# Kernel tuning notes

Measured on AMD Instinct MI355X. Metric: run time of the kernel, lower is better.

The kernel has to match this reference:

```python
import jax, jax.numpy as jnp
import numpy as np

CUTOFF = 5.0
N_RBF = 20

A = 50000
F = 128
E = 500000


def setup_inputs() -> dict:
    key = jax.random.key(0)
    ks = jax.random.split(key, 10)
    return {
        "vectors": jax.random.normal(ks[0], (A, 3, F), dtype=jnp.float32),
        "scalars": jax.random.normal(ks[1], (A, 1, F), dtype=jnp.float32),
        "directions": jax.random.normal(ks[2], (E, 3), dtype=jnp.float32),
        "idx_i": jax.random.randint(ks[3], (E,), 0, A),
        "idx_j": jax.random.randint(ks[4], (E,), 0, A),
        "W1": jax.random.normal(ks[5], (F, F), dtype=jnp.float32) / np.sqrt(F),
        "b1": jnp.zeros((F,), dtype=jnp.float32),
        "W2": jax.random.normal(ks[6], (F, 3 * F), dtype=jnp.float32) / np.sqrt(F),
        "b2": jnp.zeros((3 * F,), dtype=jnp.float32),
        "Wr": jax.random.normal(ks[7], (N_RBF, 3 * F), dtype=jnp.float32) / np.sqrt(N_RBF),
        "br": jnp.zeros((3 * F,), dtype=jnp.float32),
    }


def reference(vectors, scalars, directions, idx_i, idx_j, W1, b1, W2, b2, Wr, br):
    feat = scalars.shape[-1]
    n_nodes = vectors.shape[0]
    n_rbf = Wr.shape[0]

    s = jax.nn.silu(scalars @ W1 + b1) @ W2 + b2

    # edge norms: E x 1
    norm_r = jnp.sqrt(jnp.sum(directions * directions, axis=-1, keepdims=True))

    # radial basis: sin(k*pi/rc * |r|)/|r|  -> E x n
    rr = jnp.arange(1, n_rbf + 1, dtype=directions.dtype)
    rbf = jnp.sin(rr * (jnp.pi / CUTOFF) * norm_r) / norm_r
    r = rbf @ Wr + br  # E x 3F

    # cosine cutoff with hard mask (min(delta,0)/delta == 1 inside cutoff, 0 outside)
    delta = norm_r - CUTOFF
    mask = jnp.minimum(delta, 0.0) / delta
    fc = 0.5 * (jnp.cos(jnp.pi * norm_r / CUTOFF) + 1.0) * mask
    r = fc * r  # E x 3F

    combined = s[idx_i] * r[:, None, :]
    delta_s, delta_v1, delta_v2 = jnp.split(combined, 3, axis=-1)

    delta_v = vectors[idx_i] * delta_v1 + delta_v2 * (directions / norm_r)[:, :, None]

    # scatter-add back to nodes
    delta_s = jax.ops.segment_sum(delta_s, idx_j, num_segments=n_nodes)
    delta_v = jax.ops.segment_sum(delta_v, idx_j, num_segments=n_nodes)
    return delta_v, delta_s
```

## Files before the change

kernel.cpp:

```cpp
#include <hip/hip_runtime.h>
#include <math.h>

#define A_NODES 50000
#define FEAT 128
#define EDGES 500000
#define NRBF 20
#define CUTOFF_F 5.0f
#define PI_OVER_CUTOFF 0.6283185307179586f

typedef unsigned int uint32;
typedef unsigned short ushort16;
typedef short bf16x8 __attribute__((ext_vector_type(8)));
typedef float f32x4 __attribute__((ext_vector_type(4)));
typedef float f32x2 __attribute__((ext_vector_type(2)));

__device__ __forceinline__ ushort16 f2bf(float f) {
    union { float f; uint32 u; } v; v.f = f;
    uint32 r = (v.u + 0x7fffu + ((v.u >> 16) & 1u)) >> 16;
    return (ushort16)r;
}
__device__ __forceinline__ uint32 packbf(float a, float b) {
    return (uint32)f2bf(a) | ((uint32)f2bf(b) << 16);
}
__device__ __forceinline__ float bf_lo(uint32 u) { return __uint_as_float(u << 16); }
__device__ __forceinline__ float bf_hi(uint32 u) { return __uint_as_float(u & 0xffff0000u); }

#if __has_builtin(__builtin_amdgcn_fdot2_f32_bf16)
typedef __bf16 bf16x2 __attribute__((ext_vector_type(2)));
__device__ __forceinline__ float dot2(uint32 a, uint32 b, float c) {
    return __builtin_amdgcn_fdot2_f32_bf16(
        __builtin_bit_cast(bf16x2, a), __builtin_bit_cast(bf16x2, b), c, false);
}
#else
__device__ __forceinline__ float dot2(uint32 a, uint32 b, float c) {
    return fmaf(bf_hi(a), bf_hi(b), fmaf(bf_lo(a), bf_lo(b), c));
}
#endif

__global__ __launch_bounds__(256) void pack_kernel(
    const float* __restrict__ W1, const float* __restrict__ W2,
    const float* __restrict__ Wr,
    ushort16* __restrict__ w1pk, ushort16* __restrict__ w2pk,
    uint32* __restrict__ wrpk)
{
    const int t = blockIdx.x * 256 + threadIdx.x;
    if (t < 16384) {
        const int jj = t & 7, l = (t >> 3) & 63, kk = (t >> 9) & 3, nt = t >> 11;
        const int col = (l & 15) + 16 * nt;
        const int k   = kk * 32 + (l >> 4) * 8 + jj;
        w1pk[t] = f2bf(W1[k * 128 + col]);
    } else if (t < 16384 + 49152) {
        const int u = t - 16384;
        const int jj = u & 7, l = (u >> 3) & 63, kk = (u >> 9) & 3, nt = u >> 11;
        const int col = (l & 15) + 16 * nt;
        const int k   = kk * 32 + (l >> 4) * 8 + jj;
        w2pk[u] = f2bf(W2[k * 384 + col]);
    } else if (t < 16384 + 49152 + 3840) {
        const int u = t - 16384 - 49152;
        const int m = u / 384, col = u % 384;
        wrpk[u] = packbf(Wr[(2 * m) * 384 + col], Wr[(2 * m + 1) * 384 + col]);
    }
}

__global__ __launch_bounds__(256) void node_mlp_kernel(
    const float* __restrict__ scalars,
    const ushort16* __restrict__ w1pk, const float* __restrict__ bias1,
    const ushort16* __restrict__ w2pk, const float* __restrict__ bias2,
    ushort16* __restrict__ s_bf)
{
    __shared__ ushort16 sc[16][136];
    __shared__ ushort16 hd[16][136];
    const int tx   = threadIdx.x;
    const int lane = tx & 63;
    const int wv   = tx >> 6;
    const int base = blockIdx.x * 16;

    {
        const int row = tx >> 4;
        const int cs  = (tx & 15) * 8;
        const float* src = scalars + (size_t)(base + row) * FEAT + cs;
        const float4 f0 = *(const float4*)src;
        const float4 f1 = *(const float4*)(src + 4);
        bf16x8 tmp;
        tmp[0] = (short)f2bf(f0.x); tmp[1] = (short)f2bf(f0.y);
        tmp[2] = (short)f2bf(f0.z); tmp[3] = (short)f2bf(f0.w);
        tmp[4] = (short)f2bf(f1.x); tmp[5] = (short)f2bf(f1.y);
        tmp[6] = (short)f2bf(f1.z); tmp[7] = (short)f2bf(f1.w);
        *(bf16x8*)&sc[row][cs] = tmp;
    }
    __syncthreads();

    const int arow = lane & 15;
    const int kgrp = lane >> 4;

    f32x4 acc0 = {0.f, 0.f, 0.f, 0.f};
    f32x4 acc1 = {0.f, 0.f, 0.f, 0.f};
    #pragma unroll
    for (int kk = 0; kk < 4; ++kk) {
        const bf16x8 a  = *(const bf16x8*)&sc[arow][kk * 32 + kgrp * 8];
        const bf16x8 b0 = *(const bf16x8*)(w1pk + (((size_t)(wv * 2 + 0) * 4 + kk) * 64 + lane) * 8);
        const bf16x8 b1 = *(const bf16x8*)(w1pk + (((size_t)(wv * 2 + 1) * 4 + kk) * 64 + lane) * 8);
        acc0 = __builtin_amdgcn_mfma_f32_16x16x32_bf16(a, b0, acc0, 0, 0, 0);
        acc1 = __builtin_amdgcn_mfma_f32_16x16x32_bf16(a, b1, acc1, 0, 0, 0);
    }
    {
        const int c0 = wv * 32 + (lane & 15);
        const int c1 = c0 + 16;
        const float bb0 = bias1[c0], bb1 = bias1[c1];
        #pragma unroll
        for (int r = 0; r < 4; ++r) {
            const int row = kgrp * 4 + r;
            float x0 = acc0[r] + bb0;
            float x1 = acc1[r] + bb1;
            x0 = x0 / (1.0f + __expf(-x0));
            x1 = x1 / (1.0f + __expf(-x1));
            hd[row][c0] = f2bf(x0);
            hd[row][c1] = f2bf(x1);
        }
    }
    __syncthreads();

    f32x4 acc[6];
    #pragma unroll
    for (int n = 0; n < 6; ++n) acc[n] = (f32x4){0.f, 0.f, 0.f, 0.f};
    #pragma unroll
    for (int kk = 0; kk < 4; ++kk) {
        const bf16x8 a = *(const bf16x8*)&hd[arow][kk * 32 + kgrp * 8];
        #pragma unroll
        for (int n = 0; n < 6; ++n) {
            const bf16x8 b = *(const bf16x8*)(w2pk + (((size_t)(wv * 6 + n) * 4 + kk) * 64 + lane) * 8);
            acc[n] = __builtin_amdgcn_mfma_f32_16x16x32_bf16(a, b, acc[n], 0, 0, 0);
        }
    }
    #pragma unroll
    for (int n = 0; n < 6; ++n) {
        const int col = (wv * 6 + n) * 16 + (lane & 15);
        const float bb = bias2[col];
        #pragma unroll
        for (int r = 0; r < 4; ++r) {
            const int row = kgrp * 4 + r;
            s_bf[(size_t)(base + row) * 384 + col] = f2bf(acc[n][r] + bb);
        }
    }
}

__global__ __launch_bounds__(256) void vec_cvt_kernel(
    const float* __restrict__ vin, uint32* __restrict__ vbf)
{
    const int t = blockIdx.x * 256 + threadIdx.x;
    const size_t n2 = (size_t)A_NODES * 384 / 2;
    if (t < (int)n2) {
        const float a = vin[2 * (size_t)t];
        const float b = vin[2 * (size_t)t + 1];
        vbf[t] = packbf(a, b);
    }
}

__global__ __launch_bounds__(256) void hist_kernel(
    const int* __restrict__ idx_j, int* __restrict__ hist)
{
    const int e = blockIdx.x * 256 + threadIdx.x;
    if (e < EDGES) atomicAdd(&hist[idx_j[e]], 1);
}

__global__ __launch_bounds__(1024) void scan_kernel(
    const int* __restrict__ hist, int* __restrict__ offsets,
    int* __restrict__ cursor)
{
    __shared__ int part[1024];
    const int t = threadIdx.x;
    const int CH = (A_NODES + 1023) / 1024;

    int sum = 0;
    for (int k = 0; k < CH; ++k) {
        const int idx = t * CH + k;
        if (idx < A_NODES) sum += hist[idx];
    }
    part[t] = sum;
    __syncthreads();
    for (int off = 1; off < 1024; off <<= 1) {
        const int v = (t >= off) ? part[t - off] : 0;
        __syncthreads();
        part[t] += v;
        __syncthreads();
    }
    int run = part[t] - sum;
    for (int k = 0; k < CH; ++k) {
        const int idx = t * CH + k;
        if (idx < A_NODES) {
            offsets[idx] = run;
            cursor[idx]  = run;
            run += hist[idx];
        }
    }
    if (t == 0) offsets[A_NODES] = EDGES;
}

__global__ __launch_bounds__(256) void edge_prep_kernel(
    const float* __restrict__ directions,
    const int* __restrict__ idx_i, const int* __restrict__ idx_j,
    int* __restrict__ cursor,
    float* __restrict__ edata)
{
    const int e = blockIdx.x * 256 + threadIdx.x;
    if (e >= EDGES) return;
    const int j   = idx_j[e];
    const int pos = atomicAdd(&cursor[j], 1);
    const int i   = idx_i[e];
    const float d0 = directions[(size_t)e * 3 + 0];
    const float d1 = directions[(size_t)e * 3 + 1];
    const float d2 = directions[(size_t)e * 3 + 2];
    const float nr   = sqrtf(d0 * d0 + d1 * d1 + d2 * d2);
    const float invn = 1.0f / nr;
    const float x = PI_OVER_CUTOFF * nr;
    float sx, cx;
    sincosf(x, &sx, &cx);
    const float fc = (nr < CUTOFF_F) ? 0.5f * (cx + 1.0f) : 0.0f;
    const float scale = invn * fc;
    const float twoc = 2.0f * cx;

    float out16[16];
    float s_odd = sx;
    float s_prev = 0.0f;
    #pragma unroll
    for (int m = 0; m < 10; ++m) {
        const float s_even = twoc * s_odd - s_prev;
        out16[m] = __uint_as_float(packbf(s_odd * scale, s_even * scale));
        const float s_next = twoc * s_even - s_odd;
        s_prev = s_even;
        s_odd  = s_next;
    }
    out16[10] = d0 * invn;
    out16[11] = d1 * invn;
    out16[12] = d2 * invn;
    out16[13] = fc;
    out16[14] = __int_as_float(i);
    out16[15] = 0.0f;

    float4* dst = (float4*)(edata + (size_t)pos * 16);
    dst[0] = make_float4(out16[0],  out16[1],  out16[2],  out16[3]);
    dst[1] = make_float4(out16[4],  out16[5],  out16[6],  out16[7]);
    dst[2] = make_float4(out16[8],  out16[9],  out16[10], out16[11]);
    dst[3] = make_float4(out16[12], out16[13], out16[14], out16[15]);
}

template <int VBF>
__global__ __launch_bounds__(256, 4) void gather_kernel(
    const ushort16* __restrict__ s_bf,
    const ushort16* __restrict__ v_bf,
    const float* __restrict__ vectors_f32,
    const uint32* __restrict__ wrpk, const float* __restrict__ br,
    const float* __restrict__ edata,
    const int* __restrict__ offsets,
    float* __restrict__ out_v, float* __restrict__ out_s)
{
    const int lane = threadIdx.x & 63;
    const int wv   = __builtin_amdgcn_readfirstlane(threadIdx.x >> 6);
    const int j    = blockIdx.x;
    const int c0   = lane * 2;

    const int beg = offsets[j];
    const int end = offsets[j + 1];

    float accsA = 0.f, accsB = 0.f;
    float avA0 = 0.f, avA1 = 0.f, avA2 = 0.f;
    float avB0 = 0.f, avB1 = 0.f, avB2 = 0.f;

    uint32 wA[30], wB[30];
    float brA0 = 0.f, brB0 = 0.f, brA1 = 0.f, brB1 = 0.f, brA2 = 0.f, brB2 = 0.f;

    int p = beg + wv;
    float4 cA, cB, cC, cD;

    if (p < end) {
        #pragma unroll
        for (int s = 0; s < 3; ++s)
            #pragma unroll
            for (int m = 0; m < 10; ++m) {
                wA[s * 10 + m] = wrpk[m * 384 + s * 128 + c0];
                wB[s * 10 + m] = wrpk[m * 384 + s * 128 + c0 + 1];
            }
        brA0 = br[c0];       brB0 = br[c0 + 1];
        brA1 = br[128 + c0]; brB1 = br[129 + c0];
        brA2 = br[256 + c0]; brB2 = br[257 + c0];

        const float4* s0p = (const float4*)(edata + (size_t)p * 16);
        cA = s0p[0]; cB = s0p[1]; cC = s0p[2]; cD = s0p[3];
    }

    while (p < end) {
        const int pn = p + 4;
        const int i  = __float_as_int(cD.z);

        const ushort16* srow = s_bf + (size_t)i * 384;
        const uint32 s0 = *(const uint32*)(srow + c0);
        const uint32 s1 = *(const uint32*)(srow + 128 + c0);
        const uint32 s2 = *(const uint32*)(srow + 256 + c0);

        float vA0, vB0, vA1, vB1, vA2, vB2;
        if (VBF) {
            const ushort16* vrow = v_bf + (size_t)i * 384;
            const uint32 v0 = *(const uint32*)(vrow + c0);
            const uint32 v1 = *(const uint32*)(vrow + 128 + c0);
            const uint32 v2 = *(const uint32*)(vrow + 256 + c0);
            vA0 = bf_lo(v0); vB0 = bf_hi(v0);
            vA1 = bf_lo(v1); vB1 = bf_hi(v1);
            vA2 = bf_lo(v2); vB2 = bf_hi(v2);
        } else {
            const float* vrow = vectors_f32 + (size_t)i * 384;
            vA0 = vrow[c0];       vB0 = vrow[c0 + 1];
            vA1 = vrow[128 + c0]; vB1 = vrow[129 + c0];
            vA2 = vrow[256 + c0]; vB2 = vrow[257 + c0];
        }

        const size_t pf = (size_t)(pn < end ? pn : p) * 16;
        const float4* sn = (const float4*)(edata + pf);
        const float4 nA = sn[0], nB = sn[1], nC = sn[2], nD = sn[3];

        const float u0 = cC.z, u1 = cC.w, u2 = cD.x;
        const float fcv = cD.y;

        uint32 rb[10] = {
            __float_as_uint(cA.x), __float_as_uint(cA.y),
            __float_as_uint(cA.z), __float_as_uint(cA.w),
            __float_as_uint(cB.x), __float_as_uint(cB.y),
            __float_as_uint(cB.z), __float_as_uint(cB.w),
            __float_as_uint(cC.x), __float_as_uint(cC.y) };

        float rA0 = fcv * brA0, rA1 = fcv * brA1, rA2 = fcv * brA2;
        float rB0 = fcv * brB0, rB1 = fcv * brB1, rB2 = fcv * brB2;
        #pragma unroll
        for (int m = 0; m < 10; ++m) {
            const uint32 rm = rb[m];
            rA0 = dot2(rm, wA[m],      rA0);
            rA1 = dot2(rm, wA[10 + m], rA1);
            rA2 = dot2(rm, wA[20 + m], rA2);
            rB0 = dot2(rm, wB[m],      rB0);
            rB1 = dot2(rm, wB[10 + m], rB1);
            rB2 = dot2(rm, wB[20 + m], rB2);
        }

        const float sA0 = bf_lo(s0), sB0 = bf_hi(s0);
        const float sA1 = bf_lo(s1), sB1 = bf_hi(s1);
        const float sA2 = bf_lo(s2), sB2 = bf_hi(s2);

        accsA = fmaf(sA0, rA0, accsA);
        accsB = fmaf(sB0, rB0, accsB);
        const float gA1 = sA1 * rA1, gA2 = sA2 * rA2;
        const float gB1 = sB1 * rB1, gB2 = sB2 * rB2;

        avA0 = fmaf(vA0, gA1, fmaf(gA2, u0, avA0));
        avB0 = fmaf(vB0, gB1, fmaf(gB2, u0, avB0));
        avA1 = fmaf(vA1, gA1, fmaf(gA2, u1, avA1));
        avB1 = fmaf(vB1, gB1, fmaf(gB2, u1, avB1));
        avA2 = fmaf(vA2, gA1, fmaf(gA2, u2, avA2));
        avB2 = fmaf(vB2, gB1, fmaf(gB2, u2, avB2));

        cA = nA; cB = nB; cC = nC; cD = nD;
        p = pn;
    }

    __shared__ float red[4][64][9];
    float* slot = red[wv][lane];
    slot[0] = accsA; slot[1] = accsB;
    slot[2] = avA0;  slot[3] = avB0;
    slot[4] = avA1;  slot[5] = avB1;
    slot[6] = avA2;  slot[7] = avB2;
    __syncthreads();

    if (wv == 0) {
        const float* o1 = red[1][lane];
        const float* o2 = red[2][lane];
        const float* o3 = red[3][lane];
        f32x2 t;
        t.x = accsA + o1[0] + o2[0] + o3[0];
        t.y = accsB + o1[1] + o2[1] + o3[1];
        __builtin_nontemporal_store(t, (f32x2*)(out_s + (size_t)j * 128 + c0));
        float* ov = out_v + (size_t)j * 384;
        t.x = avA0 + o1[2] + o2[2] + o3[2];
        t.y = avB0 + o1[3] + o2[3] + o3[3];
        __builtin_nontemporal_store(t, (f32x2*)(ov + c0));
        t.x = avA1 + o1[4] + o2[4] + o3[4];
        t.y = avB1 + o1[5] + o2[5] + o3[5];
        __builtin_nontemporal_store(t, (f32x2*)(ov + 128 + c0));
        t.x = avA2 + o1[6] + o2[6] + o3[6];
        t.y = avB2 + o1[7] + o2[7] + o3[7];
        __builtin_nontemporal_store(t, (f32x2*)(ov + 256 + c0));
    }
}

extern "C" void kernel_launch(void* const* d_in, const int* in_sizes, int n_in,
                              void* d_out, int out_size, void* d_ws, size_t ws_size,
                              hipStream_t stream) {
    const float* vectors    = (const float*)d_in[0];
    const float* scalars    = (const float*)d_in[1];
    const float* directions = (const float*)d_in[2];
    const int*   idx_i      = (const int*)d_in[3];
    const int*   idx_j      = (const int*)d_in[4];
    const float* W1         = (const float*)d_in[5];
    const float* b1         = (const float*)d_in[6];
    const float* W2         = (const float*)d_in[7];
    const float* b2         = (const float*)d_in[8];
    const float* Wr         = (const float*)d_in[9];
    const float* br         = (const float*)d_in[10];

    float* out_v = (float*)d_out;
    float* out_s = out_v + (size_t)A_NODES * 3 * FEAT;

    char* ws = (char*)d_ws;
    ushort16* s_bf = (ushort16*)ws;  ws += (size_t)A_NODES * 384 * 2;
    float* edata   = (float*)ws;     ws += (size_t)EDGES * 16 * 4;
    uint32* wrpk   = (uint32*)ws;    ws += (size_t)10 * 384 * 4;
    ushort16* w1pk = (ushort16*)ws;  ws += (size_t)16384 * 2;
    ushort16* w2pk = (ushort16*)ws;  ws += (size_t)49152 * 2;
    int* hist      = (int*)ws;       ws += (size_t)A_NODES * 4;
    int* offsets   = (int*)ws;       ws += (((size_t)(A_NODES + 1) * 4 + 15) & ~(size_t)15);
    int* cursor    = (int*)ws;       ws += (size_t)A_NODES * 4;
    ushort16* v_bf = (ushort16*)ws;  ws += (size_t)A_NODES * 384 * 2;

    const int use_vbf = ((size_t)(ws - (char*)d_ws) <= ws_size) ? 1 : 0;

    hipMemsetAsync(hist, 0, (size_t)A_NODES * 4, stream);

    pack_kernel<<<271, 256, 0, stream>>>(W1, W2, Wr, w1pk, w2pk, wrpk);
    node_mlp_kernel<<<A_NODES / 16, 256, 0, stream>>>(scalars, w1pk, b1, w2pk, b2, s_bf);
    if (use_vbf)
        vec_cvt_kernel<<<(A_NODES * 384 / 2 + 255) / 256, 256, 0, stream>>>(vectors, (uint32*)v_bf);

    hist_kernel<<<(EDGES + 255) / 256, 256, 0, stream>>>(idx_j, hist);
    scan_kernel<<<1, 1024, 0, stream>>>(hist, offsets, cursor);
    edge_prep_kernel<<<(EDGES + 255) / 256, 256, 0, stream>>>(
        directions, idx_i, idx_j, cursor, edata);

    if (use_vbf)
        gather_kernel<1><<<A_NODES, 256, 0, stream>>>(
            s_bf, v_bf, vectors, wrpk, br, edata, offsets, out_v, out_s);
    else
        gather_kernel<0><<<A_NODES, 256, 0, stream>>>(
            s_bf, v_bf, vectors, wrpk, br, edata, offsets, out_v, out_s);
}
```

Measured before the change: 613.2 us.

## Assign one wavefront per destination node and vectorize bf16 conversion

The gather kernel now maps each wavefront to its own destination node (four nodes per block) instead of splitting a node's edges across four waves. This removes the shared-memory reduction and the __syncthreads. Weight loads become vectorized uint2 and are hoisted ahead of the edge loop. The vector-to-bf16 conversion kernel is widened to process eight floats per thread with float4 loads and uint4 stores. The trade-off is a longer serial edge chain per wave and more load imbalance between waves of a block, since nodes have different degrees.

```diff
diff --git a/kernel.cpp b/kernel.cpp
--- a/kernel.cpp
+++ b/kernel.cpp
@@ -145,14 +145,17 @@
 }
 
 __global__ __launch_bounds__(256) void vec_cvt_kernel(
-    const float* __restrict__ vin, uint32* __restrict__ vbf)
-{
-    const int t = blockIdx.x * 256 + threadIdx.x;
-    const size_t n2 = (size_t)A_NODES * 384 / 2;
-    if (t < (int)n2) {
-        const float a = vin[2 * (size_t)t];
-        const float b = vin[2 * (size_t)t + 1];
-        vbf[t] = packbf(a, b);
+    const float* __restrict__ vin, uint4* __restrict__ vbf)
+{
+    const size_t t = (size_t)blockIdx.x * 256 + threadIdx.x;
+    const size_t n8 = (size_t)A_NODES * 384 / 8;
+    if (t < n8) {
+        const float4 f0 = ((const float4*)vin)[2 * t];
+        const float4 f1 = ((const float4*)vin)[2 * t + 1];
+        uint4 o;
+        o.x = packbf(f0.x, f0.y); o.y = packbf(f0.z, f0.w);
+        o.z = packbf(f1.x, f1.y); o.w = packbf(f1.z, f1.w);
+        vbf[t] = o;
     }
 }
 
@@ -255,9 +258,21 @@
     float* __restrict__ out_v, float* __restrict__ out_s)
 {
     const int lane = threadIdx.x & 63;
-    const int wv   = __builtin_amdgcn_readfirstlane(threadIdx.x >> 6);
-    const int j    = blockIdx.x;
+    const int wv   = threadIdx.x >> 6;
+    const int j    = blockIdx.x * 4 + wv;
     const int c0   = lane * 2;
+
+#define LDW(s, m) (*(const uint2*)(wrpk + (m) * 384 + (s) * 128 + c0))
+    const uint2 w00 = LDW(0,0), w01 = LDW(0,1), w02 = LDW(0,2), w03 = LDW(0,3), w04 = LDW(0,4);
+    const uint2 w05 = LDW(0,5), w06 = LDW(0,6), w07 = LDW(0,7), w08 = LDW(0,8), w09 = LDW(0,9);
+    const uint2 w10 = LDW(1,0), w11 = LDW(1,1), w12 = LDW(1,2), w13 = LDW(1,3), w14 = LDW(1,4);
+    const uint2 w15 = LDW(1,5), w16 = LDW(1,6), w17 = LDW(1,7), w18 = LDW(1,8), w19 = LDW(1,9);
+    const uint2 w20 = LDW(2,0), w21 = LDW(2,1), w22 = LDW(2,2), w23 = LDW(2,3), w24 = LDW(2,4);
+    const uint2 w25 = LDW(2,5), w26 = LDW(2,6), w27 = LDW(2,7), w28 = LDW(2,8), w29 = LDW(2,9);
+#undef LDW
+    const float2 brv0 = *(const float2*)(br + c0);
+    const float2 brv1 = *(const float2*)(br + 128 + c0);
+    const float2 brv2 = *(const float2*)(br + 256 + c0);
 
     const int beg = offsets[j];
     const int end = offsets[j + 1];
@@ -266,30 +281,15 @@
     float avA0 = 0.f, avA1 = 0.f, avA2 = 0.f;
     float avB0 = 0.f, avB1 = 0.f, avB2 = 0.f;
 
-    uint32 wA[30], wB[30];
-    float brA0 = 0.f, brB0 = 0.f, brA1 = 0.f, brB1 = 0.f, brA2 = 0.f, brB2 = 0.f;
-
-    int p = beg + wv;
+    int p = beg;
     float4 cA, cB, cC, cD;
-
     if (p < end) {
-        #pragma unroll
-        for (int s = 0; s < 3; ++s)
-            #pragma unroll
-            for (int m = 0; m < 10; ++m) {
-                wA[s * 10 + m] = wrpk[m * 384 + s * 128 + c0];
-                wB[s * 10 + m] = wrpk[m * 384 + s * 128 + c0 + 1];
-            }
-        brA0 = br[c0];       brB0 = br[c0 + 1];
-        brA1 = br[128 + c0]; brB1 = br[129 + c0];
-        brA2 = br[256 + c0]; brB2 = br[257 + c0];
-
         const float4* s0p = (const float4*)(edata + (size_t)p * 16);
         cA = s0p[0]; cB = s0p[1]; cC = s0p[2]; cD = s0p[3];
     }
 
     while (p < end) {
-        const int pn = p + 4;
+        const int pn = p + 1;
         const int i  = __float_as_int(cD.z);
 
         const ushort16* srow = s_bf + (size_t)i * 384;
@@ -317,28 +317,32 @@
         const float4* sn = (const float4*)(edata + pf);
         const float4 nA = sn[0], nB = sn[1], nC = sn[2], nD = sn[3];
 
-        const float u0 = cC.z, u1 = cC.w, u2 = cD.x;
-        const float fcv = cD.y;
-
-        uint32 rb[10] = {
-            __float_as_uint(cA.x), __float_as_uint(cA.y),
-            __float_as_uint(cA.z), __float_as_uint(cA.w),
-            __float_as_uint(cB.x), __float_as_uint(cB.y),
-            __float_as_uint(cB.z), __float_as_uint(cB.w),
-            __float_as_uint(cC.x), __float_as_uint(cC.y) };
-
-        float rA0 = fcv * brA0, rA1 = fcv * brA1, rA2 = fcv * brA2;
-        float rB0 = fcv * brB0, rB1 = fcv * brB1, rB2 = fcv * brB2;
-        #pragma unroll
-        for (int m = 0; m < 10; ++m) {
-            const uint32 rm = rb[m];
-            rA0 = dot2(rm, wA[m],      rA0);
-            rA1 = dot2(rm, wA[10 + m], rA1);
-            rA2 = dot2(rm, wA[20 + m], rA2);
-            rB0 = dot2(rm, wB[m],      rB0);
-            rB1 = dot2(rm, wB[10 + m], rB1);
-            rB2 = dot2(rm, wB[20 + m], rB2);
-        }
+        const uint32 b0 = __float_as_uint(cA.x), b1 = __float_as_uint(cA.y);
+        const uint32 b2 = __float_as_uint(cA.z), b3 = __float_as_uint(cA.w);
+        const uint32 b4 = __float_as_uint(cB.x), b5 = __float_as_uint(cB.y);
+        const uint32 b6 = __float_as_uint(cB.z), b7 = __float_as_uint(cB.w);
+        const uint32 b8 = __float_as_uint(cC.x), b9 = __float_as_uint(cC.y);
+        const float u0 = cC.z, u1 = cC.w, u2 = cD.x, fcv = cD.y;
+
+        float rA0 = fcv * brv0.x, rB0 = fcv * brv0.y;
+        float rA1 = fcv * brv1.x, rB1 = fcv * brv1.y;
+        float rA2 = fcv * brv2.x, rB2 = fcv * brv2.y;
+
+#define DOTS(bb, wa, wb, wc) \
+        rA0 = dot2(bb, wa.x, rA0); rB0 = dot2(bb, wa.y, rB0); \
+        rA1 = dot2(bb, wb.x, rA1); rB1 = dot2(bb, wb.y, rB1); \
+        rA2 = dot2(bb, wc.x, rA2); rB2 = dot2(bb, wc.y, rB2);
+        DOTS(b0, w00, w10, w20)
+        DOTS(b1, w01, w11, w21)
+        DOTS(b2, w02, w12, w22)
+        DOTS(b3, w03, w13, w23)
+        DOTS(b4, w04, w14, w24)
+        DOTS(b5, w05, w15, w25)
+        DOTS(b6, w06, w16, w26)
+        DOTS(b7, w07, w17, w27)
+        DOTS(b8, w08, w18, w28)
+        DOTS(b9, w09, w19, w29)
+#undef DOTS
 
         const float sA0 = bf_lo(s0), sB0 = bf_hi(s0);
         const float sA1 = bf_lo(s1), sB1 = bf_hi(s1);
@@ -360,33 +364,16 @@
         p = pn;
     }
 
-    __shared__ float red[4][64][9];
-    float* slot = red[wv][lane];
-    slot[0] = accsA; slot[1] = accsB;
-    slot[2] = avA0;  slot[3] = avB0;
-    slot[4] = avA1;  slot[5] = avB1;
-    slot[6] = avA2;  slot[7] = avB2;
-    __syncthreads();
-
-    if (wv == 0) {
-        const float* o1 = red[1][lane];
-        const float* o2 = red[2][lane];
-        const float* o3 = red[3][lane];
-        f32x2 t;
-        t.x = accsA + o1[0] + o2[0] + o3[0];
-        t.y = accsB + o1[1] + o2[1] + o3[1];
-        __builtin_nontemporal_store(t, (f32x2*)(out_s + (size_t)j * 128 + c0));
-        float* ov = out_v + (size_t)j * 384;
-        t.x = avA0 + o1[2] + o2[2] + o3[2];
-        t.y = avB0 + o1[3] + o2[3] + o3[3];
-        __builtin_nontemporal_store(t, (f32x2*)(ov + c0));
-        t.x = avA1 + o1[4] + o2[4] + o3[4];
-        t.y = avB1 + o1[5] + o2[5] + o3[5];
-        __builtin_nontemporal_store(t, (f32x2*)(ov + 128 + c0));
-        t.x = avA2 + o1[6] + o2[6] + o3[6];
-        t.y = avB2 + o1[7] + o2[7] + o3[7];
-        __builtin_nontemporal_store(t, (f32x2*)(ov + 256 + c0));
-    }
+    f32x2 t;
+    t.x = accsA; t.y = accsB;
+    __builtin_nontemporal_store(t, (f32x2*)(out_s + (size_t)j * 128 + c0));
+    float* ov = out_v + (size_t)j * 384;
+    t.x = avA0; t.y = avB0;
+    __builtin_nontemporal_store(t, (f32x2*)(ov + c0));
+    t.x = avA1; t.y = avB1;
+    __builtin_nontemporal_store(t, (f32x2*)(ov + 128 + c0));
+    t.x = avA2; t.y = avB2;
+    __builtin_nontemporal_store(t, (f32x2*)(ov + 256 + c0));
 }
 
 extern "C" void kernel_launch(void* const* d_in, const int* in_sizes, int n_in,
@@ -425,7 +412,8 @@
     pack_kernel<<<271, 256, 0, stream>>>(W1, W2, Wr, w1pk, w2pk, wrpk);
     node_mlp_kernel<<<A_NODES / 16, 256, 0, stream>>>(scalars, w1pk, b1, w2pk, b2, s_bf);
     if (use_vbf)
-        vec_cvt_kernel<<<(A_NODES * 384 / 2 + 255) / 256, 256, 0, stream>>>(vectors, (uint32*)v_bf);
+        vec_cvt_kernel<<<(int)(((size_t)A_NODES * 384 / 8 + 255) / 256), 256, 0, stream>>>(
+            vectors, (uint4*)v_bf);
 
     hist_kernel<<<(EDGES + 255) / 256, 256, 0, stream>>>(idx_j, hist);
     scan_kernel<<<1, 1024, 0, stream>>>(hist, offsets, cursor);
@@ -433,9 +421,9 @@
         directions, idx_i, idx_j, cursor, edata);
 
     if (use_vbf)
-        gather_kernel<1><<<A_NODES, 256, 0, stream>>>(
+        gather_kernel<1><<<A_NODES / 4, 256, 0, stream>>>(
             s_bf, v_bf, vectors, wrpk, br, edata, offsets, out_v, out_s);
     else
-        gather_kernel<0><<<A_NODES, 256, 0, stream>>>(
+        gather_kernel<0><<<A_NODES / 4, 256, 0, stream>>>(
             s_bf, v_bf, vectors, wrpk, br, edata, offsets, out_v, out_s);
 }
```

Result: faster. 571.6 us (-6.8%).
